# Kernel tuning notes

Measured on AMD Instinct MI355X. Metric: run time of the kernel, lower is better.

Reference implementation:

```python
import jax, jax.numpy as jnp
import numpy as np

N_NODES = 100000
N_EDGES = 3200000
PERIODS = 12
C_IN, C_OUT, F_OUT = 1, 4, 12


def setup_inputs() -> dict:
    key = jax.random.key(0)
    ks = jax.random.split(key, 20)
    s = 0.1
    return {
        "x": jax.random.normal(ks[0], (N_NODES, C_IN, PERIODS), dtype=jnp.float32),
        "edge_index": jax.random.randint(ks[1], (2, N_EDGES), 0, N_NODES, dtype=jnp.int32),
        "conv_z_w": s * jax.random.normal(ks[2], (C_IN, C_OUT), dtype=jnp.float32),
        "conv_z_b": s * jax.random.normal(ks[3], (C_OUT,), dtype=jnp.float32),
        "lin_z_w": s * jax.random.normal(ks[4], (2 * C_OUT, C_OUT), dtype=jnp.float32),
        "lin_z_b": s * jax.random.normal(ks[5], (C_OUT,), dtype=jnp.float32),
        "conv_r_w": s * jax.random.normal(ks[6], (C_IN, C_OUT), dtype=jnp.float32),
        "conv_r_b": s * jax.random.normal(ks[7], (C_OUT,), dtype=jnp.float32),
        "lin_r_w": s * jax.random.normal(ks[8], (2 * C_OUT, C_OUT), dtype=jnp.float32),
        "lin_r_b": s * jax.random.normal(ks[9], (C_OUT,), dtype=jnp.float32),
        "conv_h_w": s * jax.random.normal(ks[10], (C_IN, C_OUT), dtype=jnp.float32),
        "conv_h_b": s * jax.random.normal(ks[11], (C_OUT,), dtype=jnp.float32),
        "lin_h_w": s * jax.random.normal(ks[12], (2 * C_OUT, C_OUT), dtype=jnp.float32),
        "lin_h_b": s * jax.random.normal(ks[13], (C_OUT,), dtype=jnp.float32),
        "att": jax.random.normal(ks[14], (PERIODS,), dtype=jnp.float32),
        "out_w": s * jax.random.normal(ks[15], (C_OUT, F_OUT), dtype=jnp.float32),
        "out_b": s * jax.random.normal(ks[16], (F_OUT,), dtype=jnp.float32),
        "f": 12,
    }


def reference(x, edge_index, conv_z_w, conv_z_b, lin_z_w, lin_z_b,
              conv_r_w, conv_r_b, lin_r_w, lin_r_b,
              conv_h_w, conv_h_b, lin_h_w, lin_h_b,
              att, out_w, out_b, f):
    N, _, P = x.shape
    loops = jnp.arange(N, dtype=edge_index.dtype)
    src = jnp.concatenate([edge_index[0], loops])  # self loops, fill=1
    dst = jnp.concatenate([edge_index[1], loops])
    deg = jax.ops.segment_sum(jnp.ones_like(src, dtype=x.dtype), dst, num_segments=N)
    dinv = jnp.where(deg > 0, jax.lax.rsqrt(deg), 0.0)
    norm = dinv[src] * dinv[dst]  # [E+N] symmetric GCN normalization

    def gcn(xt, W, b):
        xw = xt @ W  # [N, C_OUT]
        msg = xw[src] * norm[:, None]
        return jax.ops.segment_sum(msg, dst, num_segments=N) + b

    H0 = jnp.zeros((N, conv_z_w.shape[1]), dtype=x.dtype)

    def tgcn_step(xt):  # xt: [N, C_IN]; A3TGCN does not carry H across periods
        z = jax.nn.sigmoid(jnp.concatenate([gcn(xt, conv_z_w, conv_z_b), H0], 1) @ lin_z_w + lin_z_b)
        r = jax.nn.sigmoid(jnp.concatenate([gcn(xt, conv_r_w, conv_r_b), H0], 1) @ lin_r_w + lin_r_b)
        h_t = jnp.tanh(jnp.concatenate([gcn(xt, conv_h_w, conv_h_b), r * H0], 1) @ lin_h_w + lin_h_b)
        return z * H0 + (1.0 - z) * h_t

    xs = jnp.transpose(x, (2, 0, 1))  # [P, N, C_IN]
    Hs = jax.vmap(tgcn_step)(xs)  # [P, N, C_OUT]
    probs = jax.nn.softmax(att)
    H_accum = jnp.einsum('p,pnd->nd', probs, Hs)  # attention over periods
    out = H_accum @ out_w + out_b  # [N, 12]
    return out[:, :f]
```

## Files before the change

kernel.cpp:

```cpp
#include <hip/hip_runtime.h>
#include <hip/hip_fp16.h>
#include <math.h>


#define PERIODS 12
#define BSZ     256
#define BSH     8
#define HALF    128
#define STRIDE  9216
#define SCAP    4800
#define SRCBITS 17
#define SMASK   ((1 << SRCBITS) - 1)
#define CH      4096

struct Consts {
    float az[4], cz[4], ah[4], ch[4], probs[PERIODS];
};

typedef float vf2 __attribute__((ext_vector_type(2)));

__device__ __forceinline__ float dec1_manual(unsigned b) {
    unsigned e = (b >> 3) & 15u, m = b & 7u;
    float v = e ? __uint_as_float(((e + 120u) << 23) | (m << 20))
                : (float)m * 0.001953125f;
    return (b & 0x80u) ? -v : v;
}

__device__ __forceinline__ void dec4(unsigned u, float* o) {
#if __has_builtin(__builtin_amdgcn_cvt_pk_f32_fp8)
    vf2 lo = __builtin_amdgcn_cvt_pk_f32_fp8((int)u, false);
    vf2 hi = __builtin_amdgcn_cvt_pk_f32_fp8((int)u, true);
    o[0] = lo.x; o[1] = lo.y; o[2] = hi.x; o[3] = hi.y;
#else
    o[0] = dec1_manual(u & 255u);
    o[1] = dec1_manual((u >> 8) & 255u);
    o[2] = dec1_manual((u >> 16) & 255u);
    o[3] = dec1_manual(u >> 24);
#endif
}

__device__ __forceinline__ unsigned enc1_manual(float x) {
    unsigned s = (__float_as_uint(x) >> 24) & 0x80u;
    float a = fabsf(x);
    if (!(a > 0.f)) return s;
    a = fminf(a, 448.f);
    int eb = (int)(__float_as_uint(a) >> 23) - 127;
    int e = eb < -6 ? -6 : eb;
    float q = rintf(a * exp2f((float)(3 - e)));
    if (q >= 16.f) { e++; q = rintf(a * exp2f((float)(3 - e))); }
    if (e > 8) return s | 0x7Eu;
    int m = (int)q;
    unsigned ee, mm;
    if (m >= 8) { ee = (unsigned)(e + 7); mm = (unsigned)(m - 8); }
    else        { ee = 0u; mm = (unsigned)m; }
    return s | (ee << 3) | mm;
}

__device__ __forceinline__ unsigned pk4(float a, float b, float c, float d) {
#if __has_builtin(__builtin_amdgcn_cvt_pk_fp8_f32)
    int v = __builtin_amdgcn_cvt_pk_fp8_f32(a, b, 0, false);
    v = __builtin_amdgcn_cvt_pk_fp8_f32(c, d, v, true);
    return (unsigned)v;
#else
    return enc1_manual(a) | (enc1_manual(b) << 8) |
           (enc1_manual(c) << 16) | (enc1_manual(d) << 24);
#endif
}


__global__ __launch_bounds__(512) void k_setup(const float* conv_z_w, const float* conv_z_b,
                        const float* lin_z_w, const float* lin_z_b,
                        const float* conv_h_w, const float* conv_h_b,
                        const float* lin_h_w, const float* lin_h_b,
                        const float* att, Consts* C, int* gcur, int NB,
                        unsigned short* deg16, int N, int NPAD)
{
    int t = threadIdx.x;
    for (int i = t; i < NB; i += 512) gcur[i] = 0;
    for (int i = N + t; i < NPAD; i += 512) deg16[i] = 0;
    if (t == 0) {
        for (int c = 0; c < 4; ++c) {
            float az = 0.f, cz = 0.f, ah = 0.f, ch = 0.f;
            for (int k = 0; k < 4; ++k) {
                az += conv_z_w[k] * lin_z_w[k * 4 + c];
                cz += conv_z_b[k] * lin_z_w[k * 4 + c];
                ah += conv_h_w[k] * lin_h_w[k * 4 + c];
                ch += conv_h_b[k] * lin_h_w[k * 4 + c];
            }
            C->az[c] = az; C->cz[c] = cz + lin_z_b[c];
            C->ah[c] = ah; C->ch[c] = ch + lin_h_b[c];
        }
        float m = att[0];
        for (int p = 1; p < PERIODS; ++p) m = fmaxf(m, att[p]);
        float e[PERIODS]; float s = 0.f;
        for (int p = 0; p < PERIODS; ++p) { e[p] = expf(att[p] - m); s += e[p]; }
        for (int p = 0; p < PERIODS; ++p) C->probs[p] = e[p] / s;
    }
}

__global__ __launch_bounds__(512) void k_binA(const int* __restrict__ ei,
                                              int* __restrict__ gcur,
                                              int* __restrict__ binned, int E) {
    __shared__ int hist[512];
    __shared__ int scn[512];
    __shared__ int gdel[512];
    __shared__ int sv[CH];
    __shared__ int sa[CH];
    int t = threadIdx.x;
    hist[t] = 0;
    __syncthreads();
    int base = blockIdx.x * CH;
    int lim = min(E - base, CH);
    #pragma unroll
    for (int k = 0; k < CH / 512; ++k) {
        int i = t + k * 512;
        if (i < lim) atomicAdd(&hist[ei[E + base + i] >> BSH], 1);
    }
    __syncthreads();
    int v = hist[t];
    scn[t] = v;
    __syncthreads();
    for (int off = 1; off < 512; off <<= 1) {
        int tmp = (t >= off) ? scn[t - off] : 0;
        __syncthreads();
        scn[t] += tmp;
        __syncthreads();
    }
    int excl = scn[t] - v;
    int g = (v > 0) ? atomicAdd(&gcur[t], v) : 0;
    gdel[t] = t * STRIDE + g - excl;
    hist[t] = excl;
    __syncthreads();
    #pragma unroll
    for (int k = 0; k < CH / 512; ++k) {
        int i = t + k * 512;
        if (i < lim) {
            int s = ei[base + i];
            int d = ei[E + base + i];
            int b = d >> BSH;
            int pos = atomicAdd(&hist[b], 1);
            sv[pos] = ((d & (BSZ - 1)) << SRCBITS) | s;
            sa[pos] = gdel[b] + pos;
        }
    }
    __syncthreads();
    for (int j = t; j < lim; j += 512)
        binned[sa[j]] = sv[j];
}

__global__ __launch_bounds__(512) void k_prep(const int* __restrict__ binned,
                                              const int* __restrict__ gcur,
                                              const float* __restrict__ x,
                                              unsigned short* __restrict__ deg16,
                                              uint4* __restrict__ xs8, int N) {
    __shared__ int ldeg[BSZ];
    int b = blockIdx.x, t = threadIdx.x;
    if (t < BSZ) ldeg[t] = 0;
    __syncthreads();
    int cnt = gcur[b];
    const int* bb = binned + b * STRIDE;
    for (int i = t; i < cnt; i += 512)
        atomicAdd(&ldeg[bb[i] >> SRCBITS], 1);
    __syncthreads();
    if (t < BSZ) {
        int n = (b << BSH) + t;
        if (n < N) {
            int dg = ldeg[t];
            deg16[n] = (unsigned short)dg;
            float di = rsqrtf((float)dg + 1.0f);
            const float4* xv = (const float4*)(x + (size_t)n * PERIODS);
            float4 v0 = xv[0], v1 = xv[1], v2 = xv[2];
            uint4 r;
            r.x = pk4(v0.x * di, v0.y * di, v0.z * di, v0.w * di);
            r.y = pk4(v1.x * di, v1.y * di, v1.z * di, v1.w * di);
            r.z = pk4(v2.x * di, v2.y * di, v2.z * di, v2.w * di);
            r.w = 0;
            xs8[n] = r;
        }
    }
}

__device__ __forceinline__ void accdec(float* acc, uint4 r) {
    float f[PERIODS];
    dec4(r.x, f + 0); dec4(r.y, f + 4); dec4(r.z, f + 8);
    #pragma unroll
    for (int k = 0; k < PERIODS; ++k) acc[k] += f[k];
}

__global__ __launch_bounds__(512) void k_agg(const int* __restrict__ binned,
                                             const int* __restrict__ gcur,
                                             const unsigned short* __restrict__ deg16,
                                             const uint4* __restrict__ xs8,
                                             const Consts* __restrict__ C,
                                             const float* __restrict__ out_w,
                                             const float* __restrict__ out_b,
                                             float* __restrict__ out, int N) {
    __shared__ int ofs[HALF + 1];
    __shared__ int cur[HALF];
    __shared__ int scn[HALF];
    __shared__ int sorted[SCAP];
    int t = threadIdx.x;
    int b = blockIdx.x >> 1;
    int halfSel = blockIdx.x & 1;
    int nbase = (b << BSH) + halfSel * HALF;

    int d = 0;
    if (t < HALF) { d = deg16[nbase + t]; scn[t] = d; }
    __syncthreads();
    for (int off = 1; off < HALF; off <<= 1) {
        int v = (t < HALF && t >= off) ? scn[t - off] : 0;
        __syncthreads();
        if (t < HALF) scn[t] += v;
        __syncthreads();
    }
    if (t < HALF) { int e = scn[t] - d; ofs[t] = e; cur[t] = e; }
    if (t == HALF - 1) ofs[HALF] = scn[HALF - 1];
    __syncthreads();

    int cnt = gcur[b];
    const int* bb = binned + b * STRIDE;
    for (int i = t; i < cnt; i += 512) {
        int v = bb[i];
        int dl = v >> SRCBITS;
        if ((dl >> 7) == halfSel) {
            int pos = atomicAdd(&cur[dl & (HALF - 1)], 1);
            sorted[pos] = v & SMASK;
        }
    }
    __syncthreads();

    int ln = t >> 2;
    int lane = t & 3;
    int start = ofs[ln];
    int end = ofs[ln + 1];

    float acc[PERIODS];
    #pragma unroll
    for (int k = 0; k < PERIODS; ++k) acc[k] = 0.f;

    int i = start + lane;
    for (; i + 4 < end; i += 8) {
        int s0 = sorted[i];
        int s1 = sorted[i + 4];
        uint4 r0 = xs8[s0];
        uint4 r1 = xs8[s1];
        accdec(acc, r0);
        accdec(acc, r1);
    }
    if (i < end) {
        uint4 r0 = xs8[sorted[i]];
        accdec(acc, r0);
    }

    #pragma unroll
    for (int k = 0; k < PERIODS; ++k) {
        acc[k] += __shfl_xor(acc[k], 1);
        acc[k] += __shfl_xor(acc[k], 2);
    }

    int gn = nbase + ln;
    if (lane != 0 || gn >= N) return;

    {
        float f[PERIODS];
        uint4 r = xs8[gn];
        dec4(r.x, f + 0); dec4(r.y, f + 4); dec4(r.z, f + 8);
        #pragma unroll
        for (int k = 0; k < PERIODS; ++k) acc[k] += f[k];
    }

    float di = rsqrtf((float)(end - start) + 1.0f);
    float hacc[4] = {0.f, 0.f, 0.f, 0.f};
    #pragma unroll
    for (int p = 0; p < PERIODS; ++p) {
        float ap = di * acc[p];
        float pr = C->probs[p];
        #pragma unroll
        for (int c = 0; c < 4; ++c) {
            float zz = 1.f / (1.f + __expf(-(ap * C->az[c] + C->cz[c])));
            float hh = tanhf(ap * C->ah[c] + C->ch[c]);
            hacc[c] += pr * (1.f - zz) * hh;
        }
    }
    float o[PERIODS];
    #pragma unroll
    for (int f = 0; f < PERIODS; ++f) {
        float v = out_b[f];
        #pragma unroll
        for (int c = 0; c < 4; ++c) v += hacc[c] * out_w[c * PERIODS + f];
        o[f] = v;
    }
    float4* ov = (float4*)(out + (size_t)gn * PERIODS);
    ov[0] = make_float4(o[0], o[1], o[2],  o[3]);
    ov[1] = make_float4(o[4], o[5], o[6],  o[7]);
    ov[2] = make_float4(o[8], o[9], o[10], o[11]);
}

extern "C" void kernel_launch(void* const* d_in, const int* in_sizes, int n_in,
                              void* d_out, int out_size, void* d_ws, size_t ws_size,
                              hipStream_t stream) {
    const float* x        = (const float*)d_in[0];
    const int*   ei       = (const int*)d_in[1];
    const float* conv_z_w = (const float*)d_in[2];
    const float* conv_z_b = (const float*)d_in[3];
    const float* lin_z_w  = (const float*)d_in[4];
    const float* lin_z_b  = (const float*)d_in[5];
    const float* conv_h_w = (const float*)d_in[10];
    const float* conv_h_b = (const float*)d_in[11];
    const float* lin_h_w  = (const float*)d_in[12];
    const float* lin_h_b  = (const float*)d_in[13];
    const float* att      = (const float*)d_in[14];
    const float* out_w    = (const float*)d_in[15];
    const float* out_b    = (const float*)d_in[16];
    float* out = (float*)d_out;

    const int N    = in_sizes[0] / PERIODS;
    const int E    = in_sizes[1] / 2;
    const int NB   = (N + BSZ - 1) / BSZ;
    const int NPAD = NB * BSZ;
    const int gA   = (E + CH - 1) / CH;

    char* ws = (char*)d_ws;
    size_t off = 0;
    Consts*         consts = (Consts*)(ws + off);          off += (sizeof(Consts) + 255) & ~255ull;
    int*            gcur   = (int*)(ws + off);             off += ((size_t)NB * 4 + 255) & ~255ull;
    unsigned short* deg16  = (unsigned short*)(ws + off);  off += ((size_t)NPAD * 2 + 255) & ~255ull;
    uint4*          xs8    = (uint4*)(ws + off);           off += ((size_t)NPAD * 16 + 255) & ~255ull;
    int*            binned = (int*)(ws + off);             off += ((size_t)NB * STRIDE * 4 + 255) & ~255ull;
    (void)ws_size; (void)n_in; (void)out_size;

    k_setup<<<1, 512, 0, stream>>>(conv_z_w, conv_z_b, lin_z_w, lin_z_b,
                                   conv_h_w, conv_h_b, lin_h_w, lin_h_b, att,
                                   consts, gcur, NB, deg16, N, NPAD);
    k_binA<<<gA, 512, 0, stream>>>(ei, gcur, binned, E);
    k_prep<<<NB, 512, 0, stream>>>(binned, gcur, x, deg16, xs8, N);
    k_agg<<<NB * 2, 512, 0, stream>>>(binned, gcur, deg16, xs8, consts,
                                      out_w, out_b, out, N);
}
```

Baseline: 185.9 us.

## Bin edges into 128-node superbins and scatter directly without block scan

Edges are binned by destination into 128-node superbins instead of 256-node bins. Each binning block now scatters directly from registers using shared-atomic positions, with no prefix scan or shared-memory staging. The aggregation and prep kernels then read only their own superbin, so neither reads edges that belong to the other half. The cost is less coalesced global scatter writes and more bins contending on the global counters.

```diff
diff --git a/kernel.cpp b/kernel.cpp
--- a/kernel.cpp
+++ b/kernel.cpp
@@ -4,11 +4,8 @@
 
 
 #define PERIODS 12
-#define BSZ     256
-#define BSH     8
 #define HALF    128
-#define STRIDE  9216
-#define SCAP    4800
+#define STRIDE2 4800
 #define SRCBITS 17
 #define SMASK   ((1 << SRCBITS) - 1)
 #define CH      4096
@@ -72,11 +69,11 @@
                         const float* lin_z_w, const float* lin_z_b,
                         const float* conv_h_w, const float* conv_h_b,
                         const float* lin_h_w, const float* lin_h_b,
-                        const float* att, Consts* C, int* gcur, int NB,
+                        const float* att, Consts* C, int* gcur, int NSB,
                         unsigned short* deg16, int N, int NPAD)
 {
     int t = threadIdx.x;
-    for (int i = t; i < NB; i += 512) gcur[i] = 0;
+    for (int i = t; i < NSB; i += 512) gcur[i] = 0;
     for (int i = N + t; i < NPAD; i += 512) deg16[i] = 0;
     if (t == 0) {
         for (int c = 0; c < 4; ++c) {
@@ -101,69 +98,60 @@
 __global__ __launch_bounds__(512) void k_binA(const int* __restrict__ ei,
                                               int* __restrict__ gcur,
                                               int* __restrict__ binned, int E) {
-    __shared__ int hist[512];
-    __shared__ int scn[512];
-    __shared__ int gdel[512];
-    __shared__ int sv[CH];
-    __shared__ int sa[CH];
+    __shared__ int hist[1024];
+    __shared__ int gdel[1024];
     int t = threadIdx.x;
-    hist[t] = 0;
+    hist[t] = 0; hist[t + 512] = 0;
     __syncthreads();
     int base = blockIdx.x * CH;
     int lim = min(E - base, CH);
+    int pv[CH / 512];
+    int meta[CH / 512];
     #pragma unroll
     for (int k = 0; k < CH / 512; ++k) {
         int i = t + k * 512;
-        if (i < lim) atomicAdd(&hist[ei[E + base + i] >> BSH], 1);
-    }
-    __syncthreads();
-    int v = hist[t];
-    scn[t] = v;
-    __syncthreads();
-    for (int off = 1; off < 512; off <<= 1) {
-        int tmp = (t >= off) ? scn[t - off] : 0;
-        __syncthreads();
-        scn[t] += tmp;
-        __syncthreads();
-    }
-    int excl = scn[t] - v;
-    int g = (v > 0) ? atomicAdd(&gcur[t], v) : 0;
-    gdel[t] = t * STRIDE + g - excl;
-    hist[t] = excl;
-    __syncthreads();
-    #pragma unroll
-    for (int k = 0; k < CH / 512; ++k) {
-        int i = t + k * 512;
+        pv[k] = -1;
         if (i < lim) {
             int s = ei[base + i];
             int d = ei[E + base + i];
-            int b = d >> BSH;
-            int pos = atomicAdd(&hist[b], 1);
-            sv[pos] = ((d & (BSZ - 1)) << SRCBITS) | s;
-            sa[pos] = gdel[b] + pos;
-        }
-    }
-    __syncthreads();
-    for (int j = t; j < lim; j += 512)
-        binned[sa[j]] = sv[j];
-}
-
-__global__ __launch_bounds__(512) void k_prep(const int* __restrict__ binned,
+            int sb = d >> 7;
+            int pos = atomicAdd(&hist[sb], 1);
+            pv[k] = ((d & (HALF - 1)) << SRCBITS) | s;
+            meta[k] = (sb << 13) | pos;
+        }
+    }
+    __syncthreads();
+    for (int sb = t; sb < 1024; sb += 512) {
+        int h = hist[sb];
+        if (h > 0) gdel[sb] = sb * STRIDE2 + atomicAdd(&gcur[sb], h);
+    }
+    __syncthreads();
+    #pragma unroll
+    for (int k = 0; k < CH / 512; ++k) {
+        if (pv[k] >= 0) {
+            int sb = meta[k] >> 13;
+            int pos = meta[k] & 8191;
+            binned[gdel[sb] + pos] = pv[k];
+        }
+    }
+}
+
+__global__ __launch_bounds__(256) void k_prep(const int* __restrict__ binned,
                                               const int* __restrict__ gcur,
                                               const float* __restrict__ x,
                                               unsigned short* __restrict__ deg16,
                                               uint4* __restrict__ xs8, int N) {
-    __shared__ int ldeg[BSZ];
-    int b = blockIdx.x, t = threadIdx.x;
-    if (t < BSZ) ldeg[t] = 0;
-    __syncthreads();
-    int cnt = gcur[b];
-    const int* bb = binned + b * STRIDE;
-    for (int i = t; i < cnt; i += 512)
+    __shared__ int ldeg[HALF];
+    int sb = blockIdx.x, t = threadIdx.x;
+    if (t < HALF) ldeg[t] = 0;
+    __syncthreads();
+    int cnt = gcur[sb];
+    const int* bb = binned + sb * STRIDE2;
+    for (int i = t; i < cnt; i += 256)
         atomicAdd(&ldeg[bb[i] >> SRCBITS], 1);
     __syncthreads();
-    if (t < BSZ) {
-        int n = (b << BSH) + t;
+    if (t < HALF) {
+        int n = sb * HALF + t;
         if (n < N) {
             int dg = ldeg[t];
             deg16[n] = (unsigned short)dg;
@@ -198,11 +186,10 @@
     __shared__ int ofs[HALF + 1];
     __shared__ int cur[HALF];
     __shared__ int scn[HALF];
-    __shared__ int sorted[SCAP];
+    __shared__ int sorted[STRIDE2];
     int t = threadIdx.x;
-    int b = blockIdx.x >> 1;
-    int halfSel = blockIdx.x & 1;
-    int nbase = (b << BSH) + halfSel * HALF;
+    int sb = blockIdx.x;
+    int nbase = sb * HALF;
 
     int d = 0;
     if (t < HALF) { d = deg16[nbase + t]; scn[t] = d; }
@@ -217,15 +204,12 @@
     if (t == HALF - 1) ofs[HALF] = scn[HALF - 1];
     __syncthreads();
 
-    int cnt = gcur[b];
-    const int* bb = binned + b * STRIDE;
+    int cnt = gcur[sb];
+    const int* bb = binned + sb * STRIDE2;
     for (int i = t; i < cnt; i += 512) {
         int v = bb[i];
-        int dl = v >> SRCBITS;
-        if ((dl >> 7) == halfSel) {
-            int pos = atomicAdd(&cur[dl & (HALF - 1)], 1);
-            sorted[pos] = v & SMASK;
-        }
+        int pos = atomicAdd(&cur[v >> SRCBITS], 1);
+        sorted[pos] = v & SMASK;
     }
     __syncthreads();
 
@@ -316,24 +300,24 @@
 
     const int N    = in_sizes[0] / PERIODS;
     const int E    = in_sizes[1] / 2;
-    const int NB   = (N + BSZ - 1) / BSZ;
-    const int NPAD = NB * BSZ;
+    const int NSB  = (N + HALF - 1) / HALF;
+    const int NPAD = NSB * HALF;
     const int gA   = (E + CH - 1) / CH;
 
     char* ws = (char*)d_ws;
     size_t off = 0;
     Consts*         consts = (Consts*)(ws + off);          off += (sizeof(Consts) + 255) & ~255ull;
-    int*            gcur   = (int*)(ws + off);             off += ((size_t)NB * 4 + 255) & ~255ull;
+    int*            gcur   = (int*)(ws + off);             off += ((size_t)NSB * 4 + 255) & ~255ull;
     unsigned short* deg16  = (unsigned short*)(ws + off);  off += ((size_t)NPAD * 2 + 255) & ~255ull;
     uint4*          xs8    = (uint4*)(ws + off);           off += ((size_t)NPAD * 16 + 255) & ~255ull;
-    int*            binned = (int*)(ws + off);             off += ((size_t)NB * STRIDE * 4 + 255) & ~255ull;
+    int*            binned = (int*)(ws + off);             off += ((size_t)NSB * STRIDE2 * 4 + 255) & ~255ull;
     (void)ws_size; (void)n_in; (void)out_size;
 
     k_setup<<<1, 512, 0, stream>>>(conv_z_w, conv_z_b, lin_z_w, lin_z_b,
                                    conv_h_w, conv_h_b, lin_h_w, lin_h_b, att,
-                                   consts, gcur, NB, deg16, N, NPAD);
+                                   consts, gcur, NSB, deg16, N, NPAD);
     k_binA<<<gA, 512, 0, stream>>>(ei, gcur, binned, E);
-    k_prep<<<NB, 512, 0, stream>>>(binned, gcur, x, deg16, xs8, N);
-    k_agg<<<NB * 2, 512, 0, stream>>>(binned, gcur, deg16, xs8, consts,
-                                      out_w, out_b, out, N);
-}
+    k_prep<<<NSB, 256, 0, stream>>>(binned, gcur, x, deg16, xs8, N);
+    k_agg<<<NSB, 512, 0, stream>>>(binned, gcur, deg16, xs8, consts,
+                                   out_w, out_b, out, N);
+}
```

Result: slower. 191.2 us (+2.8%).

## Simplify edge binning: record per-edge slot, drop scan and LDS staging

Applied to the files above, without the earlier changes.

The binning kernel now records each edge's local slot within its bucket during the histogram pass and stores it in a 16-bit shared array. This removes the block-wide prefix scan and the LDS staging buffers. The second pass writes each edge directly to its global binned position instead of through a coalesced shared-memory copy. The chunk size doubles, halving the block count and the global atomics per bucket. In exchange the global writes are scattered rather than contiguous, and ei is read twice.

```diff
diff --git a/kernel.cpp b/kernel.cpp
--- a/kernel.cpp
+++ b/kernel.cpp
@@ -11,7 +11,7 @@
 #define SCAP    4800
 #define SRCBITS 17
 #define SMASK   ((1 << SRCBITS) - 1)
-#define CH      4096
+#define CH      8192
 
 struct Consts {
     float az[4], cz[4], ah[4], ch[4], probs[PERIODS];
@@ -101,11 +101,9 @@
 __global__ __launch_bounds__(512) void k_binA(const int* __restrict__ ei,
                                               int* __restrict__ gcur,
                                               int* __restrict__ binned, int E) {
+    __shared__ unsigned short pos16[CH];
     __shared__ int hist[512];
-    __shared__ int scn[512];
     __shared__ int gdel[512];
-    __shared__ int sv[CH];
-    __shared__ int sa[CH];
     int t = threadIdx.x;
     hist[t] = 0;
     __syncthreads();
@@ -114,22 +112,17 @@
     #pragma unroll
     for (int k = 0; k < CH / 512; ++k) {
         int i = t + k * 512;
-        if (i < lim) atomicAdd(&hist[ei[E + base + i] >> BSH], 1);
-    }
-    __syncthreads();
-    int v = hist[t];
-    scn[t] = v;
-    __syncthreads();
-    for (int off = 1; off < 512; off <<= 1) {
-        int tmp = (t >= off) ? scn[t - off] : 0;
-        __syncthreads();
-        scn[t] += tmp;
-        __syncthreads();
-    }
-    int excl = scn[t] - v;
-    int g = (v > 0) ? atomicAdd(&gcur[t], v) : 0;
-    gdel[t] = t * STRIDE + g - excl;
-    hist[t] = excl;
+        if (i < lim) {
+            int d = ei[E + base + i];
+            int p = atomicAdd(&hist[d >> BSH], 1);
+            pos16[i] = (unsigned short)p;
+        }
+    }
+    __syncthreads();
+    {
+        int h = hist[t];
+        if (h > 0) gdel[t] = t * STRIDE + atomicAdd(&gcur[t], h);
+    }
     __syncthreads();
     #pragma unroll
     for (int k = 0; k < CH / 512; ++k) {
@@ -137,15 +130,10 @@
         if (i < lim) {
             int s = ei[base + i];
             int d = ei[E + base + i];
-            int b = d >> BSH;
-            int pos = atomicAdd(&hist[b], 1);
-            sv[pos] = ((d & (BSZ - 1)) << SRCBITS) | s;
-            sa[pos] = gdel[b] + pos;
-        }
-    }
-    __syncthreads();
-    for (int j = t; j < lim; j += 512)
-        binned[sa[j]] = sv[j];
+            int sb = d >> BSH;
+            binned[gdel[sb] + (int)pos16[i]] = ((d & (BSZ - 1)) << SRCBITS) | s;
+        }
+    }
 }
 
 __global__ __launch_bounds__(512) void k_prep(const int* __restrict__ binned,
```

Result: slower. 198.1 us (+6.6%).
